# Performance work log

Hardware: AMD Instinct MI355X
Metric: run time of the kernel (lower is better)

## Reference

```python
import jax, jax.numpy as jnp
import numpy as np

KERNEL = 9
STRIDE = 2
NUM_ITERS = 3


def squash(s):
    # Matches the module: norm over last dim; v = ||s|| / (1 + ||s||^2) * s
    n = jnp.linalg.norm(s, axis=-1, keepdims=True)
    return n / (1.0 + n * n) * s


def setup_inputs() -> dict:
    key = jax.random.key(0)
    k1, k2, k3 = jax.random.split(key, 3)
    B, nc, ic, oc, H = 32, 32, 256, 32, 71  # H'=(71-9)//2+1 = 32 = B = nc = oc (required by the original broadcasting)
    x = jax.random.normal(k1, (B, ic, H, H), dtype=jnp.float32)
    # Conv2d default init: U(-1/sqrt(fan_in), 1/sqrt(fan_in)), fan_in = ic*9*9
    bound = 1.0 / np.sqrt(ic * KERNEL * KERNEL)
    W = jax.random.uniform(k2, (nc, oc, ic, KERNEL, KERNEL), jnp.float32, -bound, bound)
    b = jax.random.uniform(k3, (nc, oc), jnp.float32, -bound, bound)
    return {"x": x, "W": W, "b": b}


def reference(x, W, b):
    nc, oc, ic = W.shape[0], W.shape[1], W.shape[2]
    # All nc per-capsule convs fused into one grouped output-channel conv
    Wf = W.reshape(nc * oc, ic, KERNEL, KERNEL)
    u = jax.lax.conv_general_dilated(
        x, Wf, window_strides=(STRIDE, STRIDE), padding='VALID',
        dimension_numbers=('NCHW', 'OIHW', 'NCHW'))
    B = u.shape[0]
    Hp, Wp = u.shape[2], u.shape[3]
    u_hat = u.reshape(B, nc, oc, Hp, Wp) + b[None, :, :, None, None]  # [B,nc,oc,Hp,Wp]

    # Dynamic routing. The torch code initializes b_ij as rank-4 zeros; because
    # softmax(0) is uniform and 0 + agreement == agreement, this rank-5 zero init
    # is numerically identical and shape-clean.
    b_ij = jnp.zeros((B, nc, oc, Hp, 1), dtype=u_hat.dtype)
    v = None
    for it in range(NUM_ITERS):
        c = jax.nn.softmax(b_ij, axis=1)                  # over capsule dim
        s = (c * u_hat).sum(axis=2, keepdims=True)        # [B,nc,1,Hp,Wp]
        v = squash(s)
        if it < NUM_ITERS - 1:
            b_ij = b_ij + (u_hat * v).sum(axis=-1, keepdims=True)  # [B,nc,oc,Hp,1]
    # torch returns v_j.squeeze(-1): last dim is Wp != 1 so it is a no-op
    return v  # [B, nc, 1, Hp, Wp]
```

## Files before the change

### kernel.cpp

```cpp
#include <hip/hip_runtime.h>
#include <cstdint>
#include <cstddef>

typedef unsigned short u16;
typedef signed char s8;
typedef __attribute__((ext_vector_type(4))) int i32x4;

#define XT_HSTRIDE 18432
#define XT_BSTRIDE 1308672
#define K_TOT 20736
#define N_TOT 32768
#define NKT 324
#define S_X (5.0f / 127.0f)

__device__ __forceinline__ u16 f2bf(float f) {
  uint32_t u = __builtin_bit_cast(uint32_t, f);
  u = (u + 0x7fffu + ((u >> 16) & 1u)) >> 16;
  return (u16)u;
}
__device__ __forceinline__ float bf2f(u16 h) {
  uint32_t u = ((uint32_t)h) << 16;
  return __builtin_bit_cast(float, u);
}

__device__ __forceinline__ void gl_lds16(const s8* g, s8* l) {
  __builtin_amdgcn_global_load_lds((const __attribute__((address_space(1))) void*)g,
                                   (__attribute__((address_space(3))) void*)l, 16, 0, 0);
}

__device__ __forceinline__ void wg_barrier() {
  asm volatile("" ::: "memory");
  __builtin_amdgcn_s_barrier();
  asm volatile("" ::: "memory");
}

__device__ __forceinline__ void koffs(int kt, int& ka, int& kb) {
  const int pos = kt >> 2;
  const int cq = kt & 3;
  const int kh = pos / 9;
  const int kw = pos - kh * 9;
  ka = kt * 64;
  kb = kh * XT_HSTRIDE + (kw & 1) * 9216 + (kw >> 1) * 256 + cq * 64;
}

__global__ __launch_bounds__(256) void pack_w(const float* __restrict__ W,
                                              s8* __restrict__ Wb,
                                              float* __restrict__ sw) {
  __shared__ s8 wl[20736];
  __shared__ float red[256];
  const int m = blockIdx.x;
  const int t = threadIdx.x;
  const size_t base = (size_t)m * K_TOT;
  float mx = 0.f;
  for (int i = t; i < K_TOT; i += 256) mx = fmaxf(mx, fabsf(W[base + i]));
  red[t] = mx;
  __syncthreads();
  for (int s = 128; s > 0; s >>= 1) {
    if (t < s) red[t] = fmaxf(red[t], red[t + s]);
    __syncthreads();
  }
  const float amax = fmaxf(red[0], 1e-20f);
  const float inv = 127.0f / amax;
  if (t == 0) sw[m] = amax * (1.0f / 127.0f);
  for (int i = t; i < K_TOT; i += 256) {
    float f = W[base + i];
    int c = i / 81;
    int pos = i - c * 81;
    wl[pos * 256 + c] = (s8)__float2int_rn(f * inv);
  }
  __syncthreads();
  for (int i = t; i < K_TOT; i += 256) Wb[base + i] = wl[i];
}

__global__ __launch_bounds__(256) void pack_x(const float* __restrict__ X,
                                              s8* __restrict__ xT) {
  __shared__ s8 xl[256 * 73];
  const int h = blockIdx.x;
  const int b = blockIdx.y;
  const int t = threadIdx.x;
  for (int i = t; i < 256 * 71; i += 256) {
    int c = i / 71;
    int w = i - c * 71;
    float f = X[(((size_t)(b * 256 + c)) * 71 + h) * 71 + w];
    f = fminf(fmaxf(f, -5.f), 5.f) * 25.4f;
    xl[c * 73 + w] = (s8)__float2int_rn(f);
  }
  __syncthreads();
  const size_t obase = (size_t)b * XT_BSTRIDE + (size_t)h * XT_HSTRIDE;
  for (int s = 0; s < 71; ++s) {
    int par = (s >= 36) ? 1 : 0;
    int j = s - par * 36;
    int w = 2 * j + par;
    xT[obase + par * 9216 + j * 256 + t] = xl[t * 73 + w];
  }
}

__global__ __launch_bounds__(512, 2) void conv_gemm(const s8* __restrict__ Wb,
                                                    const s8* __restrict__ xT,
                                                    const float* __restrict__ sw,
                                                    u16* __restrict__ U) {
  __shared__ __align__(16) s8 As[2][256 * 64];
  __shared__ __align__(16) s8 Bs[2][256 * 64];
  const int tid = threadIdx.x;
  const int bx = blockIdx.x;
  const int swz = (bx & 7) * 64 + (bx >> 3);
  const int m0 = (swz & 3) * 256;
  const int n0 = (swz >> 2) * 256;
  const int lane = tid & 63;
  const int wave = tid >> 6;
  const int wm = wave >> 2;
  const int wn = wave & 3;

  const int rl2 = lane >> 2;
  const int gch16 = ((lane & 3) ^ ((rl2 >> 1) & 3)) * 16;

  const s8* aS[2];
  const s8* bS[2];
#pragma unroll
  for (int j = 0; j < 2; ++j) {
    const int row = j * 128 + wave * 16 + rl2;
    aS[j] = Wb + (size_t)(m0 + row) * K_TOT + gch16;
    const int n = n0 + row;
    const size_t nb = (size_t)(n >> 10) * XT_BSTRIDE +
                      (size_t)(((n >> 5) & 31) * 2) * XT_HSTRIDE +
                      (size_t)(n & 31) * 256;
    bS[j] = xT + nb + gch16;
  }
  const int sdst = wave * 16 * 64 + lane * 16;

  i32x4 acc[8][4];
#pragma unroll
  for (int i = 0; i < 8; ++i)
#pragma unroll
    for (int j = 0; j < 4; ++j) acc[i][j] = (i32x4){0, 0, 0, 0};

  const int fr = lane & 15;
  const int q4 = lane >> 4;
  const int cph = ((q4 ^ ((fr >> 1) & 3))) * 16;
  int offA[8], offB[4];
#pragma unroll
  for (int mi = 0; mi < 8; ++mi)
    offA[mi] = (wm * 128 + (mi & 3) * 16 + (mi >> 2) * 64 + fr) * 64 + cph;
#pragma unroll
  for (int j = 0; j < 4; ++j)
    offB[j] = (wn * 64 + j * 16 + fr) * 64 + cph;

  {
    int ka0, kb0;
    koffs(0, ka0, kb0);
    gl_lds16(bS[0] + kb0, &Bs[0][0 * 8192 + sdst]);
    gl_lds16(bS[1] + kb0, &Bs[0][1 * 8192 + sdst]);
    gl_lds16(aS[0] + ka0, &As[0][0 * 8192 + sdst]);
    gl_lds16(aS[1] + ka0, &As[0][1 * 8192 + sdst]);
  }

#pragma unroll 1
  for (int kt = 0; kt < NKT; ++kt) {
    const int p = kt & 1;
    const bool more = (kt + 1 < NKT);
    int kan = 0, kbn = 0;
    if (more) koffs(kt + 1, kan, kbn);
    s8* An = &As[p ^ 1][0];
    s8* Bn = &Bs[p ^ 1][0];
    const s8* Ac = &As[p][0];
    const s8* Bc = &Bs[p][0];

    asm volatile("s_waitcnt vmcnt(0)" ::: "memory");
    wg_barrier();

    i32x4 aF[8], bF[4];

#pragma unroll
    for (int j = 0; j < 4; ++j) bF[j] = *(const i32x4*)(Bc + offB[j]);
#pragma unroll
    for (int mi = 0; mi < 4; ++mi) aF[mi] = *(const i32x4*)(Ac + offA[mi]);
    if (more) {
      gl_lds16(bS[0] + kbn, Bn + 0 * 8192 + sdst);
      gl_lds16(bS[1] + kbn, Bn + 1 * 8192 + sdst);
    }
    __builtin_amdgcn_sched_barrier(0);

    __builtin_amdgcn_s_setprio(1);
#pragma unroll
    for (int mi = 0; mi < 4; ++mi)
#pragma unroll
      for (int j = 0; j < 4; ++j)
        acc[mi][j] = __builtin_amdgcn_mfma_i32_16x16x64_i8(aF[mi], bF[j], acc[mi][j], 0, 0, 0);
    __builtin_amdgcn_s_setprio(0);
    __builtin_amdgcn_sched_barrier(0);

#pragma unroll
    for (int mi = 4; mi < 8; ++mi) aF[mi] = *(const i32x4*)(Ac + offA[mi]);
    if (more) {
      gl_lds16(aS[0] + kan, An + 0 * 8192 + sdst);
      gl_lds16(aS[1] + kan, An + 1 * 8192 + sdst);
    }
    __builtin_amdgcn_sched_barrier(0);

    __builtin_amdgcn_s_setprio(1);
#pragma unroll
    for (int mi = 4; mi < 8; ++mi)
#pragma unroll
      for (int j = 0; j < 4; ++j)
        acc[mi][j] = __builtin_amdgcn_mfma_i32_16x16x64_i8(aF[mi], bF[j], acc[mi][j], 0, 0, 0);
    __builtin_amdgcn_s_setprio(0);
  }

  const int r0 = (lane >> 4) * 4;
  const int cn = lane & 15;
#pragma unroll
  for (int mi = 0; mi < 8; ++mi) {
    const int mgb = m0 + wm * 128 + (mi & 3) * 16 + (mi >> 2) * 64 + r0;
    float ds[4];
#pragma unroll
    for (int r = 0; r < 4; ++r) ds[r] = sw[mgb + r] * S_X;
#pragma unroll
    for (int j = 0; j < 4; ++j) {
      const int ng = n0 + wn * 64 + j * 16 + cn;
#pragma unroll
      for (int r = 0; r < 4; ++r)
        U[(size_t)(mgb + r) * N_TOT + ng] = f2bf((float)acc[mi][j][r] * ds[r]);
    }
  }
}

__global__ __launch_bounds__(1024) void routing_k(const u16* __restrict__ U,
                                                  const float* __restrict__ bias,
                                                  float* __restrict__ out) {
  const int t = threadIdx.x;
  const int bx = blockIdx.x;
  const int b = bx >> 5;
  const int hp = bx & 31;
  const int oc = t & 31;
  const int nc = t >> 5;
  __shared__ float sm[1024];

  float u_r[32];
  {
    const uint4* up4 = (const uint4*)(U + (size_t)t * N_TOT + b * 1024 + hp * 32);
    const float bs = bias[t];
#pragma unroll
    for (int i = 0; i < 4; ++i) {
      uint4 q = up4[i];
      uint32_t vv[4] = {q.x, q.y, q.z, q.w};
#pragma unroll
      for (int k = 0; k < 4; ++k) {
        u_r[i * 8 + k * 2]     = bf2f((u16)(vv[k] & 0xffffu)) + bs;
        u_r[i * 8 + k * 2 + 1] = bf2f((u16)(vv[k] >> 16)) + bs;
      }
    }
  }

  float bij = 0.f;
  float s[32];
  float scale = 0.f;

  for (int it = 0; it < 3; ++it) {
    sm[t] = bij;
    __syncthreads();
    float den = 0.f;
#pragma unroll
    for (int i = 0; i < 32; ++i) den += __expf(sm[i * 32 + oc]);
    const float c = __expf(bij) / den;
#pragma unroll
    for (int w = 0; w < 32; ++w) s[w] = c * u_r[w];
#pragma unroll
    for (int off = 1; off < 32; off <<= 1) {
#pragma unroll
      for (int w = 0; w < 32; ++w) s[w] += __shfl_xor(s[w], off, 64);
    }
    float n2 = 0.f;
#pragma unroll
    for (int w = 0; w < 32; ++w) n2 += s[w] * s[w];
    scale = sqrtf(n2) / (1.f + n2);
    if (it < 2) {
      float agr = 0.f;
#pragma unroll
      for (int w = 0; w < 32; ++w) agr += u_r[w] * s[w];
      bij += scale * agr;
    }
    __syncthreads();
  }

  float val = s[0];
#pragma unroll
  for (int i = 1; i < 32; ++i) val = (oc == i) ? s[i] : val;
  out[(size_t)((b * 32 + nc) * 32 + hp) * 32 + oc] = scale * val;
}

extern "C" void kernel_launch(void* const* d_in, const int* in_sizes, int n_in,
                              void* d_out, int out_size, void* d_ws, size_t ws_size,
                              hipStream_t stream) {
  const float* x = (const float*)d_in[0];
  const float* W = (const float*)d_in[1];
  const float* bias = (const float*)d_in[2];

  s8*    Wb = (s8*)d_ws;
  float* sw = (float*)((char*)d_ws + 21233664u);
  s8*    xT = (s8*)((char*)d_ws + 21237760u);
  u16*   U  = (u16*)((char*)d_ws + 63115264u);
  float* out = (float*)d_out;

  pack_w<<<dim3(1024), dim3(256), 0, stream>>>(W, Wb, sw);
  pack_x<<<dim3(71, 32), dim3(256), 0, stream>>>(x, xT);
  conv_gemm<<<dim3(512), dim3(512), 0, stream>>>(Wb, xT, sw, U);
  routing_k<<<dim3(1024), dim3(1024), 0, stream>>>(U, bias, out);
}
```

Measured before the change: 1.042 ms.

## Process two K-tiles per barrier in conv GEMM and vectorize packing kernels

The int8 conv GEMM main loop now stages two 64-wide K-tiles per LDS buffer, which halves the number of vmcnt waits and workgroup barriers per K step. Global-to-LDS loads for the next pair are interleaved between the four MFMA phases. LDS use doubles to 128KB per block, which may cut occupancy from the two blocks per CU declared in the launch bounds. The pack_w kernel switches to float4 loads and uint4 stores. pack_x transposes through LDS so it can write 32-bit words instead of single bytes.

```diff
diff --git a/kernel.cpp b/kernel.cpp
--- a/kernel.cpp
+++ b/kernel.cpp
@@ -46,13 +46,18 @@
 __global__ __launch_bounds__(256) void pack_w(const float* __restrict__ W,
                                               s8* __restrict__ Wb,
                                               float* __restrict__ sw) {
-  __shared__ s8 wl[20736];
+  __shared__ __align__(16) s8 wl[20736];
   __shared__ float red[256];
   const int m = blockIdx.x;
   const int t = threadIdx.x;
   const size_t base = (size_t)m * K_TOT;
+  const float4* W4 = (const float4*)(W + base);
   float mx = 0.f;
-  for (int i = t; i < K_TOT; i += 256) mx = fmaxf(mx, fabsf(W[base + i]));
+  for (int i = t; i < 5184; i += 256) {
+    float4 v = W4[i];
+    mx = fmaxf(mx, fmaxf(fmaxf(fabsf(v.x), fabsf(v.y)),
+                         fmaxf(fabsf(v.z), fabsf(v.w))));
+  }
   red[t] = mx;
   __syncthreads();
   for (int s = 128; s > 0; s >>= 1) {
@@ -69,12 +74,14 @@
     wl[pos * 256 + c] = (s8)__float2int_rn(f * inv);
   }
   __syncthreads();
-  for (int i = t; i < K_TOT; i += 256) Wb[base + i] = wl[i];
+  const uint4* s4 = (const uint4*)wl;
+  uint4* d4 = (uint4*)(Wb + base);
+  for (int i = t; i < 1296; i += 256) d4[i] = s4[i];
 }
 
 __global__ __launch_bounds__(256) void pack_x(const float* __restrict__ X,
                                               s8* __restrict__ xT) {
-  __shared__ s8 xl[256 * 73];
+  __shared__ s8 xl[71 * 260];
   const int h = blockIdx.x;
   const int b = blockIdx.y;
   const int t = threadIdx.x;
@@ -83,15 +90,18 @@
     int w = i - c * 71;
     float f = X[(((size_t)(b * 256 + c)) * 71 + h) * 71 + w];
     f = fminf(fmaxf(f, -5.f), 5.f) * 25.4f;
-    xl[c * 73 + w] = (s8)__float2int_rn(f);
+    xl[w * 260 + c] = (s8)__float2int_rn(f);
   }
   __syncthreads();
   const size_t obase = (size_t)b * XT_BSTRIDE + (size_t)h * XT_HSTRIDE;
-  for (int s = 0; s < 71; ++s) {
+  const int c4 = t & 63;
+  const int g = t >> 6;
+  for (int s = g; s < 71; s += 4) {
     int par = (s >= 36) ? 1 : 0;
     int j = s - par * 36;
     int w = 2 * j + par;
-    xT[obase + par * 9216 + j * 256 + t] = xl[t * 73 + w];
+    uint32_t d = *(const uint32_t*)&xl[w * 260 + 4 * c4];
+    *(uint32_t*)&xT[obase + par * 9216 + j * 256 + 4 * c4] = d;
   }
 }
 
@@ -99,8 +109,8 @@
                                                     const s8* __restrict__ xT,
                                                     const float* __restrict__ sw,
                                                     u16* __restrict__ U) {
-  __shared__ __align__(16) s8 As[2][256 * 64];
-  __shared__ __align__(16) s8 Bs[2][256 * 64];
+  __shared__ __align__(16) s8 As[2][2][256 * 64];
+  __shared__ __align__(16) s8 Bs[2][2][256 * 64];
   const int tid = threadIdx.x;
   const int bx = blockIdx.x;
   const int swz = (bx & 7) * 64 + (bx >> 3);
@@ -146,24 +156,36 @@
     offB[j] = (wn * 64 + j * 16 + fr) * 64 + cph;
 
   {
-    int ka0, kb0;
+    int ka0, kb0, ka1, kb1;
     koffs(0, ka0, kb0);
-    gl_lds16(bS[0] + kb0, &Bs[0][0 * 8192 + sdst]);
-    gl_lds16(bS[1] + kb0, &Bs[0][1 * 8192 + sdst]);
-    gl_lds16(aS[0] + ka0, &As[0][0 * 8192 + sdst]);
-    gl_lds16(aS[1] + ka0, &As[0][1 * 8192 + sdst]);
+    koffs(1, ka1, kb1);
+    gl_lds16(bS[0] + kb0, &Bs[0][0][0 * 8192 + sdst]);
+    gl_lds16(bS[1] + kb0, &Bs[0][0][1 * 8192 + sdst]);
+    gl_lds16(bS[0] + kb1, &Bs[0][1][0 * 8192 + sdst]);
+    gl_lds16(bS[1] + kb1, &Bs[0][1][1 * 8192 + sdst]);
+    gl_lds16(aS[0] + ka0, &As[0][0][0 * 8192 + sdst]);
+    gl_lds16(aS[1] + ka0, &As[0][0][1 * 8192 + sdst]);
+    gl_lds16(aS[0] + ka1, &As[0][1][0 * 8192 + sdst]);
+    gl_lds16(aS[1] + ka1, &As[0][1][1 * 8192 + sdst]);
   }
 
 #pragma unroll 1
-  for (int kt = 0; kt < NKT; ++kt) {
-    const int p = kt & 1;
-    const bool more = (kt + 1 < NKT);
-    int kan = 0, kbn = 0;
-    if (more) koffs(kt + 1, kan, kbn);
-    s8* An = &As[p ^ 1][0];
-    s8* Bn = &Bs[p ^ 1][0];
-    const s8* Ac = &As[p][0];
-    const s8* Bc = &Bs[p][0];
+  for (int it2 = 0; it2 < NKT / 2; ++it2) {
+    const int sp = it2 & 1;
+    const bool more = (it2 + 1 < NKT / 2);
+    int ka0n = 0, kb0n = 0, ka1n = 0, kb1n = 0;
+    if (more) {
+      koffs(2 * it2 + 2, ka0n, kb0n);
+      koffs(2 * it2 + 3, ka1n, kb1n);
+    }
+    const s8* Ac0 = &As[sp][0][0];
+    const s8* Bc0 = &Bs[sp][0][0];
+    const s8* Ac1 = &As[sp][1][0];
+    const s8* Bc1 = &Bs[sp][1][0];
+    s8* An0 = &As[sp ^ 1][0][0];
+    s8* Bn0 = &Bs[sp ^ 1][0][0];
+    s8* An1 = &As[sp ^ 1][1][0];
+    s8* Bn1 = &Bs[sp ^ 1][1][0];
 
     asm volatile("s_waitcnt vmcnt(0)" ::: "memory");
     wg_barrier();
@@ -171,15 +193,14 @@
     i32x4 aF[8], bF[4];
 
 #pragma unroll
-    for (int j = 0; j < 4; ++j) bF[j] = *(const i32x4*)(Bc + offB[j]);
-#pragma unroll
-    for (int mi = 0; mi < 4; ++mi) aF[mi] = *(const i32x4*)(Ac + offA[mi]);
-    if (more) {
-      gl_lds16(bS[0] + kbn, Bn + 0 * 8192 + sdst);
-      gl_lds16(bS[1] + kbn, Bn + 1 * 8192 + sdst);
-    }
-    __builtin_amdgcn_sched_barrier(0);
-
+    for (int j = 0; j < 4; ++j) bF[j] = *(const i32x4*)(Bc0 + offB[j]);
+#pragma unroll
+    for (int mi = 0; mi < 4; ++mi) aF[mi] = *(const i32x4*)(Ac0 + offA[mi]);
+    if (more) {
+      gl_lds16(bS[0] + kb0n, Bn0 + 0 * 8192 + sdst);
+      gl_lds16(bS[1] + kb0n, Bn0 + 1 * 8192 + sdst);
+    }
+    __builtin_amdgcn_sched_barrier(0);
     __builtin_amdgcn_s_setprio(1);
 #pragma unroll
     for (int mi = 0; mi < 4; ++mi)
@@ -190,13 +211,46 @@
     __builtin_amdgcn_sched_barrier(0);
 
 #pragma unroll
-    for (int mi = 4; mi < 8; ++mi) aF[mi] = *(const i32x4*)(Ac + offA[mi]);
-    if (more) {
-      gl_lds16(aS[0] + kan, An + 0 * 8192 + sdst);
-      gl_lds16(aS[1] + kan, An + 1 * 8192 + sdst);
-    }
-    __builtin_amdgcn_sched_barrier(0);
-
+    for (int mi = 4; mi < 8; ++mi) aF[mi] = *(const i32x4*)(Ac0 + offA[mi]);
+    if (more) {
+      gl_lds16(bS[0] + kb1n, Bn1 + 0 * 8192 + sdst);
+      gl_lds16(bS[1] + kb1n, Bn1 + 1 * 8192 + sdst);
+    }
+    __builtin_amdgcn_sched_barrier(0);
+    __builtin_amdgcn_s_setprio(1);
+#pragma unroll
+    for (int mi = 4; mi < 8; ++mi)
+#pragma unroll
+      for (int j = 0; j < 4; ++j)
+        acc[mi][j] = __builtin_amdgcn_mfma_i32_16x16x64_i8(aF[mi], bF[j], acc[mi][j], 0, 0, 0);
+    __builtin_amdgcn_s_setprio(0);
+    __builtin_amdgcn_sched_barrier(0);
+
+#pragma unroll
+    for (int j = 0; j < 4; ++j) bF[j] = *(const i32x4*)(Bc1 + offB[j]);
+#pragma unroll
+    for (int mi = 0; mi < 4; ++mi) aF[mi] = *(const i32x4*)(Ac1 + offA[mi]);
+    if (more) {
+      gl_lds16(aS[0] + ka0n, An0 + 0 * 8192 + sdst);
+      gl_lds16(aS[1] + ka0n, An0 + 1 * 8192 + sdst);
+    }
+    __builtin_amdgcn_sched_barrier(0);
+    __builtin_amdgcn_s_setprio(1);
+#pragma unroll
+    for (int mi = 0; mi < 4; ++mi)
+#pragma unroll
+      for (int j = 0; j < 4; ++j)
+        acc[mi][j] = __builtin_amdgcn_mfma_i32_16x16x64_i8(aF[mi], bF[j], acc[mi][j], 0, 0, 0);
+    __builtin_amdgcn_s_setprio(0);
+    __builtin_amdgcn_sched_barrier(0);
+
+#pragma unroll
+    for (int mi = 4; mi < 8; ++mi) aF[mi] = *(const i32x4*)(Ac1 + offA[mi]);
+    if (more) {
+      gl_lds16(aS[0] + ka1n, An1 + 0 * 8192 + sdst);
+      gl_lds16(aS[1] + ka1n, An1 + 1 * 8192 + sdst);
+    }
+    __builtin_amdgcn_sched_barrier(0);
     __builtin_amdgcn_s_setprio(1);
 #pragma unroll
     for (int mi = 4; mi < 8; ++mi)
```

Result: faster. 997.0 us (-4.3%).
